# Optimization experiments

Hardware: AMD Instinct MI355X
Metric: run time of the kernel (lower is better)

The kernel has to match this reference:

```python
import jax, jax.numpy as jnp
import numpy as np

RES = 256       # image resolution (even)
N_ANGLES = 180  # projection angles over [0, pi)
BATCH = 4


def _compute_rays(resolution):
    # Same as Radon._compute_rays: vertical chords of inscribed circle.
    s = resolution // 2
    locations = np.arange(2 * s) - s + 0.5
    ys = np.sqrt(s ** 2 - locations ** 2) + 0.5
    rays = np.stack([locations, -ys, locations, ys], axis=1)  # [R,4]
    return jnp.asarray(rays, dtype=jnp.float32)


def setup_inputs() -> dict:
    key = jax.random.key(0)
    imgs = jax.random.normal(key, (BATCH, RES, RES), dtype=jnp.float32)
    angles = jnp.linspace(0.0, np.pi, N_ANGLES, endpoint=False).astype(jnp.float32)
    rays = _compute_rays(RES)
    return {"imgs": imgs, "angles": angles, "rays": rays}


def reference(imgs, angles, rays):
    # imgs: [B,res,res]; angles: [A]; rays: [R,4] -> sinogram [B,A,R]
    res = imgs.shape[-1]
    s = res // 2
    n_steps = res  # integration samples per ray (~1px spacing across the circle)

    start = rays[:, :2]   # [R,2]
    end = rays[:, 2:]     # [R,2]
    length = jnp.sqrt(jnp.sum((end - start) ** 2, axis=-1))  # [R]

    c, sn = jnp.cos(angles), jnp.sin(angles)
    # rotation matrices [A,2,2] (CCW rotation of ray endpoints)
    rot = jnp.stack([jnp.stack([c, -sn], -1), jnp.stack([sn, c], -1)], -2)
    start_r = jnp.einsum('aij,rj->ari', rot, start)  # [A,R,2]
    end_r = jnp.einsum('aij,rj->ari', rot, end)      # [A,R,2]

    t = (jnp.arange(n_steps, dtype=jnp.float32) + 0.5) / n_steps  # [T]
    # sample points along each rotated ray: [A,R,T,2]
    pts = start_r[:, :, None, :] + t[None, None, :, None] * (end_r - start_r)[:, :, None, :]

    # world (x,y) -> continuous pixel coords (pixel centers at integer coords)
    fx = pts[..., 0] + (s - 0.5)  # [A,R,T]
    fy = pts[..., 1] + (s - 0.5)
    x0 = jnp.floor(fx)
    y0 = jnp.floor(fy)
    wx = fx - x0
    wy = fy - y0
    x0i = x0.astype(jnp.int32)
    y0i = y0.astype(jnp.int32)

    def gather(ix, iy):
        # zero-padded bilinear corner fetch, batched over imgs
        valid = (ix >= 0) & (ix < res) & (iy >= 0) & (iy < res)
        ixc = jnp.clip(ix, 0, res - 1)
        iyc = jnp.clip(iy, 0, res - 1)
        vals = imgs[:, iyc, ixc]  # [B,A,R,T]
        return jnp.where(valid[None], vals, jnp.float32(0))

    v00 = gather(x0i, y0i)
    v01 = gather(x0i + 1, y0i)
    v10 = gather(x0i, y0i + 1)
    v11 = gather(x0i + 1, y0i + 1)

    samp = (v00 * ((1 - wx) * (1 - wy))[None]
            + v01 * (wx * (1 - wy))[None]
            + v10 * ((1 - wx) * wy)[None]
            + v11 * (wx * wy)[None])  # [B,A,R,T]

    # line integral: sum of samples * step length along the ray
    sino = samp.sum(-1) * (length / n_steps)[None, None, :]  # [B,A,R]
    return sino
```

## Files before the change

kernel.cpp:

```cpp
#include <hip/hip_runtime.h>

#define RES   256
#define NANG  180
#define NRAYS 256
#define NPIX  (RES * RES)
#define OUTP  (NANG * NRAYS)

#define PITCH 258
#define PADN  (PITCH * PITCH)

#define STEEP_BLOCKS   (90 * 16)
#define SHALLOW_BLOCKS (90 * 16)
#define TOTAL_BLOCKS   (STEEP_BLOCKS + SHALLOW_BLOCKS)

#define SANG 90
#define PLANE (SANG * NRAYS)
#define PART_ELEMS (4 * 4 * PLANE)
#define RED_ELEMS  (4 * PLANE)

typedef _Float16 half2v __attribute__((ext_vector_type(2)));

__device__ __forceinline__ float hdot(unsigned int p, half2v w, float acc) {
#if __has_builtin(__builtin_amdgcn_fdot2)
    return __builtin_amdgcn_fdot2(__builtin_bit_cast(half2v, p), w, acc, false);
#else
    half2v v = __builtin_bit_cast(half2v, p);
    return acc + (float)v.x * (float)w.x + (float)v.y * (float)w.y;
#endif
}

__global__ __launch_bounds__(256) void pad_pairs(
    const float* __restrict__ imgs, uint4* __restrict__ timg)
{
    const int idx = blockIdx.x * 256 + threadIdx.x;
    if (idx >= PADN) return;
    const int y = idx / PITCH, x = idx - y * PITCH;
    const int iy = y - 1;
    const bool ry = (unsigned)iy < (unsigned)RES;
    const bool r0 = ry && ((unsigned)(x - 1) < (unsigned)RES);
    const bool r1 = ry && ((unsigned)x < (unsigned)RES);
    const int s0 = iy * RES + (x - 1);
    const int s1 = iy * RES + x;

    unsigned int u[4];
#pragma unroll
    for (int b = 0; b < 4; ++b) {
        const float v0 = r0 ? imgs[b * NPIX + s0] : 0.0f;
        const float v1 = r1 ? imgs[b * NPIX + s1] : 0.0f;
        half2v h; h.x = (_Float16)v0; h.y = (_Float16)v1;
        u[b] = __builtin_bit_cast(unsigned int, h);
    }
    timg[idx] = make_uint4(u[0], u[1], u[2], u[3]);
}

struct Geom { float srx, sry, ddx, ddy, scale; };

__device__ __forceinline__ Geom make_geom(const float* __restrict__ angles,
                                          const float* __restrict__ rays,
                                          int a, int r)
{
    float sn, cs;
    sincosf(angles[a], &sn, &cs);
    const float4 ray = reinterpret_cast<const float4*>(rays)[r];
    const float dxr = ray.z - ray.x, dyr = ray.w - ray.y;
    const float len = sqrtf(dxr * dxr + dyr * dyr);
    Geom g;
    g.srx = cs * ray.x - sn * ray.y + 127.5f;
    g.sry = sn * ray.x + cs * ray.y + 127.5f;
    g.ddx = (cs * ray.z - sn * ray.w + 127.5f) - g.srx;
    g.ddy = (sn * ray.z + cs * ray.w + 127.5f) - g.sry;
    g.scale = len * (1.0f / RES);
    return g;
}

__device__ __forceinline__ void samp2(
    const uint4* __restrict__ timg, float fx, float fy,
    float& a0, float& a1, float& a2, float& a3)
{
    const float x0f = floorf(fx), y0f = floorf(fy);
    const float wx = fx - x0f, wy = fy - y0f;

    const int idx = (int)y0f * PITCH + (int)x0f + (PITCH + 1);
    const uint4 row0 = timg[idx];
    const uint4 row1 = timg[idx + PITCH];

    const float w11 = wx * wy;
    const float w01 = wx - w11;
    const float w10 = wy - w11;
    const float w00 = (1.0f - wx) - w10;

    half2v wa; wa.x = (_Float16)w00; wa.y = (_Float16)w01;
    half2v wb; wb.x = (_Float16)w10; wb.y = (_Float16)w11;

    a0 = hdot(row0.x, wa, hdot(row1.x, wb, a0));
    a1 = hdot(row0.y, wa, hdot(row1.y, wb, a1));
    a2 = hdot(row0.z, wa, hdot(row1.z, wb, a2));
    a3 = hdot(row0.w, wa, hdot(row1.w, wb, a3));
}

__global__ __launch_bounds__(512) void radon_main(
    const uint4*  __restrict__ timg,
    const float*  __restrict__ angles,
    const float*  __restrict__ rays,
    float*        __restrict__ out,
    float*        __restrict__ part)
{
    const int bid = blockIdx.x;
    const int tid = threadIdx.x;

    if (bid < STEEP_BLOCKS) {
        const int a    = (bid >> 4) + 45;
        const int rq   = bid & 15;
        const int w    = tid >> 6;
        const int lane = tid & 63;
        const int half = lane >> 5;
        const int sub  = lane & 31;
        const int r    = rq * 16 + w * 2 + half;

        const Geom g = make_geom(angles, rays, a, r);
        float a0 = 0.f, a1 = 0.f, a2 = 0.f, a3 = 0.f;

        float fx = fmaf(((float)sub + 0.5f) * (1.0f / RES), g.ddx, g.srx);
        float fy = fmaf(((float)sub + 0.5f) * (1.0f / RES), g.ddy, g.sry);
        const float dfx = g.ddx * 0.125f;
        const float dfy = g.ddy * 0.125f;

#pragma unroll
        for (int j = 0; j < 8; ++j) {
            samp2(timg, fx, fy, a0, a1, a2, a3);
            fx += dfx; fy += dfy;
        }

#pragma unroll
        for (int m = 1; m < 32; m <<= 1) {
            a0 += __shfl_xor(a0, m, 64);
            a1 += __shfl_xor(a1, m, 64);
            a2 += __shfl_xor(a2, m, 64);
            a3 += __shfl_xor(a3, m, 64);
        }
        if (sub == 0) {
            const int base = a * NRAYS + r;
            out[0 * OUTP + base] = a0 * g.scale;
            out[1 * OUTP + base] = a1 * g.scale;
            out[2 * OUTP + base] = a2 * g.scale;
            out[3 * OUTP + base] = a3 * g.scale;
        }
    } else {
        const int b  = bid - STEEP_BLOCKS;
        const int sg = b & 3;
        const int rg = (b >> 2) & 3;
        const int as = b >> 4;
        const int a  = (as < 45) ? as : as + 90;
        const int tx = tid & 63;
        const int ty = tid >> 6;
        const int r  = rg * 64 + tx;

        const Geom g = make_geom(angles, rays, a, r);
        float a0 = 0.f, a1 = 0.f, a2 = 0.f, a3 = 0.f;

        const int k0 = sg * 64 + ty * 8;
        float fx = fmaf(((float)k0 + 0.5f) * (1.0f / RES), g.ddx, g.srx);
        float fy = fmaf(((float)k0 + 0.5f) * (1.0f / RES), g.ddy, g.sry);
        const float dfx = g.ddx * (1.0f / RES);
        const float dfy = g.ddy * (1.0f / RES);

#pragma unroll
        for (int j = 0; j < 8; ++j) {
            samp2(timg, fx, fy, a0, a1, a2, a3);
            fx += dfx; fy += dfy;
        }

        __shared__ float4 red[8][64];
        red[ty][tx] = make_float4(a0, a1, a2, a3);
        __syncthreads();

        if (ty == 0) {
#pragma unroll
            for (int j = 1; j < 8; ++j) {
                const float4 v = red[j][tx];
                a0 += v.x; a1 += v.y; a2 += v.z; a3 += v.w;
            }
            float* p = part + (size_t)sg * 4 * PLANE;
            const int base = as * NRAYS + r;
            p[0 * PLANE + base] = a0 * g.scale;
            p[1 * PLANE + base] = a1 * g.scale;
            p[2 * PLANE + base] = a2 * g.scale;
            p[3 * PLANE + base] = a3 * g.scale;
        }
    }
}

__global__ __launch_bounds__(256) void radon_reduce(
    const float* __restrict__ part, float* __restrict__ out)
{
    const int i = blockIdx.x * 256 + threadIdx.x;
    if (i >= RED_ELEMS) return;
    const int b    = i / PLANE;
    const int rest = i - b * PLANE;
    const int as   = rest >> 8;
    const int ray  = rest & 255;
    const int a    = (as < 45) ? as : as + 90;

    float s = 0.f;
#pragma unroll
    for (int sg = 0; sg < 4; ++sg)
        s += part[(sg * 4 + b) * PLANE + rest];
    out[b * OUTP + a * NRAYS + ray] = s;
}

__global__ __launch_bounds__(256) void radon_simple(
    const float* __restrict__ imgs,
    const float* __restrict__ angles,
    const float* __restrict__ rays,
    float* __restrict__ out)
{
    const int a = blockIdx.x;
    const int r = threadIdx.x;
    const Geom g = make_geom(angles, rays, a, r);
    float a0 = 0.f, a1 = 0.f, a2 = 0.f, a3 = 0.f;
    for (int k = 0; k < RES; ++k) {
        const float t  = ((float)k + 0.5f) * (1.0f / RES);
        const float fx = fmaf(t, g.ddx, g.srx);
        const float fy = fmaf(t, g.ddy, g.sry);
        const float x0f = floorf(fx), y0f = floorf(fy);
        const float wx = fx - x0f, wy = fy - y0f;
        const int x0 = (int)x0f, y0 = (int)y0f;
        const bool vx0 = (unsigned)x0 < (unsigned)RES;
        const bool vx1 = (unsigned)(x0 + 1) < (unsigned)RES;
        const bool vy0 = (unsigned)y0 < (unsigned)RES;
        const bool vy1 = (unsigned)(y0 + 1) < (unsigned)RES;
        const int x0c = min(max(x0, 0), RES - 1), x1c = min(max(x0 + 1, 0), RES - 1);
        const int y0c = min(max(y0, 0), RES - 1), y1c = min(max(y0 + 1, 0), RES - 1);
        const float omwx = 1.0f - wx, omwy = 1.0f - wy;
        const float w00 = (vx0 && vy0) ? omwx * omwy : 0.f;
        const float w01 = (vx1 && vy0) ? wx * omwy : 0.f;
        const float w10 = (vx0 && vy1) ? omwx * wy : 0.f;
        const float w11 = (vx1 && vy1) ? wx * wy : 0.f;
        const int i00 = y0c * RES + x0c, i01 = y0c * RES + x1c;
        const int i10 = y1c * RES + x0c, i11 = y1c * RES + x1c;
        a0 = fmaf(w00, imgs[i00], fmaf(w01, imgs[i01], fmaf(w10, imgs[i10], fmaf(w11, imgs[i11], a0))));
        a1 = fmaf(w00, imgs[NPIX + i00], fmaf(w01, imgs[NPIX + i01], fmaf(w10, imgs[NPIX + i10], fmaf(w11, imgs[NPIX + i11], a1))));
        a2 = fmaf(w00, imgs[2 * NPIX + i00], fmaf(w01, imgs[2 * NPIX + i01], fmaf(w10, imgs[2 * NPIX + i10], fmaf(w11, imgs[2 * NPIX + i11], a2))));
        a3 = fmaf(w00, imgs[3 * NPIX + i00], fmaf(w01, imgs[3 * NPIX + i01], fmaf(w10, imgs[3 * NPIX + i10], fmaf(w11, imgs[3 * NPIX + i11], a3))));
    }
    const int base = a * NRAYS + r;
    out[0 * OUTP + base] = a0 * g.scale;
    out[1 * OUTP + base] = a1 * g.scale;
    out[2 * OUTP + base] = a2 * g.scale;
    out[3 * OUTP + base] = a3 * g.scale;
}

extern "C" void kernel_launch(void* const* d_in, const int* in_sizes, int n_in,
                              void* d_out, int out_size, void* d_ws, size_t ws_size,
                              hipStream_t stream) {
    const float* imgs   = (const float*)d_in[0];
    const float* angles = (const float*)d_in[1];
    const float* rays   = (const float*)d_in[2];
    float* out = (float*)d_out;

    const size_t timg_bytes = (size_t)PADN * sizeof(uint4);
    const size_t need = timg_bytes + (size_t)PART_ELEMS * sizeof(float);

    if (ws_size >= need) {
        uint4* timg = (uint4*)d_ws;
        float* part = (float*)((char*)d_ws + timg_bytes);
        pad_pairs<<<(PADN + 255) / 256, 256, 0, stream>>>(imgs, timg);
        radon_main<<<TOTAL_BLOCKS, 512, 0, stream>>>(timg, angles, rays, out, part);
        radon_reduce<<<(RED_ELEMS + 255) / 256, 256, 0, stream>>>(part, out);
    } else {
        radon_simple<<<NANG, NRAYS, 0, stream>>>(imgs, angles, rays, out);
    }
}
```

Measured before the change: 35.67 us.

## Reduce shallow-angle rays fully in-block and drop the separate reduce kernel

Shallow-angle blocks now cover 32 rays each, with 16 thread rows each sampling two 8-step segments, so the whole ray sum is finished through shared memory inside one block. This removes the partial-sum workspace, its global writes and reads, and the extra radon_reduce launch. The kernel also gets a min-blocks-per-CU hint of 4 in its launch bounds. In exchange the shallow grid has half as many blocks, and each block does a heavier shared-memory reduction.

```diff
diff --git a/kernel.cpp b/kernel.cpp
--- a/kernel.cpp
+++ b/kernel.cpp
@@ -9,14 +9,9 @@
 #define PITCH 258
 #define PADN  (PITCH * PITCH)
 
+#define SHALLOW_BLOCKS (90 * 8)
 #define STEEP_BLOCKS   (90 * 16)
-#define SHALLOW_BLOCKS (90 * 16)
-#define TOTAL_BLOCKS   (STEEP_BLOCKS + SHALLOW_BLOCKS)
-
-#define SANG 90
-#define PLANE (SANG * NRAYS)
-#define PART_ELEMS (4 * 4 * PLANE)
-#define RED_ELEMS  (4 * PLANE)
+#define TOTAL_BLOCKS   (SHALLOW_BLOCKS + STEEP_BLOCKS)
 
 typedef _Float16 half2v __attribute__((ext_vector_type(2)));
 
@@ -98,19 +93,59 @@
     a3 = hdot(row0.w, wa, hdot(row1.w, wb, a3));
 }
 
-__global__ __launch_bounds__(512) void radon_main(
+__global__ __launch_bounds__(512, 4) void radon_main(
     const uint4*  __restrict__ timg,
     const float*  __restrict__ angles,
     const float*  __restrict__ rays,
-    float*        __restrict__ out,
-    float*        __restrict__ part)
+    float*        __restrict__ out)
 {
     const int bid = blockIdx.x;
     const int tid = threadIdx.x;
 
-    if (bid < STEEP_BLOCKS) {
-        const int a    = (bid >> 4) + 45;
-        const int rq   = bid & 15;
+    if (bid < SHALLOW_BLOCKS) {
+        const int as = bid >> 3;
+        const int rg = bid & 7;
+        const int a  = (as < 45) ? as : as + 90;
+        const int tx = tid & 31;
+        const int ty = tid >> 5;
+        const int r  = rg * 32 + tx;
+
+        const Geom g = make_geom(angles, rays, a, r);
+        float acc[4] = {0.f, 0.f, 0.f, 0.f};
+
+        const float dfx = g.ddx * (1.0f / RES);
+        const float dfy = g.ddy * (1.0f / RES);
+        float fx = fmaf(((float)(ty * 8) + 0.5f) * (1.0f / RES), g.ddx, g.srx);
+        float fy = fmaf(((float)(ty * 8) + 0.5f) * (1.0f / RES), g.ddy, g.sry);
+
+#pragma unroll
+        for (int sg = 0; sg < 2; ++sg) {
+#pragma unroll
+            for (int j = 0; j < 8; ++j) {
+                samp2(timg, fx, fy, acc[0], acc[1], acc[2], acc[3]);
+                fx += dfx; fy += dfy;
+            }
+            fx += g.ddx * (120.0f / RES);
+            fy += g.ddy * (120.0f / RES);
+        }
+
+        __shared__ float red[4][16][32];
+#pragma unroll
+        for (int b = 0; b < 4; ++b) red[b][ty][tx] = acc[b];
+        __syncthreads();
+
+        if (tid < 128) {
+            const int b  = tid >> 5;
+            const int t2 = tid & 31;
+            float s = 0.f;
+#pragma unroll
+            for (int j = 0; j < 16; ++j) s += red[b][j][t2];
+            out[b * OUTP + a * NRAYS + rg * 32 + t2] = s * g.scale;
+        }
+    } else {
+        const int b2   = bid - SHALLOW_BLOCKS;
+        const int a    = (b2 >> 4) + 45;
+        const int rq   = b2 & 15;
         const int w    = tid >> 6;
         const int lane = tid & 63;
         const int half = lane >> 5;
@@ -145,67 +180,7 @@
             out[2 * OUTP + base] = a2 * g.scale;
             out[3 * OUTP + base] = a3 * g.scale;
         }
-    } else {
-        const int b  = bid - STEEP_BLOCKS;
-        const int sg = b & 3;
-        const int rg = (b >> 2) & 3;
-        const int as = b >> 4;
-        const int a  = (as < 45) ? as : as + 90;
-        const int tx = tid & 63;
-        const int ty = tid >> 6;
-        const int r  = rg * 64 + tx;
-
-        const Geom g = make_geom(angles, rays, a, r);
-        float a0 = 0.f, a1 = 0.f, a2 = 0.f, a3 = 0.f;
-
-        const int k0 = sg * 64 + ty * 8;
-        float fx = fmaf(((float)k0 + 0.5f) * (1.0f / RES), g.ddx, g.srx);
-        float fy = fmaf(((float)k0 + 0.5f) * (1.0f / RES), g.ddy, g.sry);
-        const float dfx = g.ddx * (1.0f / RES);
-        const float dfy = g.ddy * (1.0f / RES);
-
-#pragma unroll
-        for (int j = 0; j < 8; ++j) {
-            samp2(timg, fx, fy, a0, a1, a2, a3);
-            fx += dfx; fy += dfy;
-        }
-
-        __shared__ float4 red[8][64];
-        red[ty][tx] = make_float4(a0, a1, a2, a3);
-        __syncthreads();
-
-        if (ty == 0) {
-#pragma unroll
-            for (int j = 1; j < 8; ++j) {
-                const float4 v = red[j][tx];
-                a0 += v.x; a1 += v.y; a2 += v.z; a3 += v.w;
-            }
-            float* p = part + (size_t)sg * 4 * PLANE;
-            const int base = as * NRAYS + r;
-            p[0 * PLANE + base] = a0 * g.scale;
-            p[1 * PLANE + base] = a1 * g.scale;
-            p[2 * PLANE + base] = a2 * g.scale;
-            p[3 * PLANE + base] = a3 * g.scale;
-        }
-    }
-}
-
-__global__ __launch_bounds__(256) void radon_reduce(
-    const float* __restrict__ part, float* __restrict__ out)
-{
-    const int i = blockIdx.x * 256 + threadIdx.x;
-    if (i >= RED_ELEMS) return;
-    const int b    = i / PLANE;
-    const int rest = i - b * PLANE;
-    const int as   = rest >> 8;
-    const int ray  = rest & 255;
-    const int a    = (as < 45) ? as : as + 90;
-
-    float s = 0.f;
-#pragma unroll
-    for (int sg = 0; sg < 4; ++sg)
-        s += part[(sg * 4 + b) * PLANE + rest];
-    out[b * OUTP + a * NRAYS + ray] = s;
+    }
 }
 
 __global__ __launch_bounds__(256) void radon_simple(
@@ -258,15 +233,12 @@
     const float* rays   = (const float*)d_in[2];
     float* out = (float*)d_out;
 
-    const size_t timg_bytes = (size_t)PADN * sizeof(uint4);
-    const size_t need = timg_bytes + (size_t)PART_ELEMS * sizeof(float);
+    const size_t need = (size_t)PADN * sizeof(uint4);
 
     if (ws_size >= need) {
         uint4* timg = (uint4*)d_ws;
-        float* part = (float*)((char*)d_ws + timg_bytes);
         pad_pairs<<<(PADN + 255) / 256, 256, 0, stream>>>(imgs, timg);
-        radon_main<<<TOTAL_BLOCKS, 512, 0, stream>>>(timg, angles, rays, out, part);
-        radon_reduce<<<(RED_ELEMS + 255) / 256, 256, 0, stream>>>(part, out);
+        radon_main<<<TOTAL_BLOCKS, 512, 0, stream>>>(timg, angles, rays, out);
     } else {
         radon_simple<<<NANG, NRAYS, 0, stream>>>(imgs, angles, rays, out);
     }
```

Result: no change. 35.05 us (-1.8%).
